# Kernel optimization log

Measured on AMD Instinct MI355X. Metric: run time of the kernel, lower is better.

The kernel has to match this reference:

```python
import jax, jax.numpy as jnp
import numpy as np

N = 20000   # nodes
E = 320000  # edges (before self-loops)
HID = 64    # hidden_dim
H = 4       # attention heads
C = HID     # per-head channels (concat=False -> mean over heads)
CDIM = 8    # contrastive_dim
NEG_SLOPE = 0.2


def setup_inputs() -> dict:
    key = jax.random.key(0)
    ks = jax.random.split(key, 32)
    g = lambda k, shape: (jax.random.normal(k, shape, jnp.float32) * 0.05)
    inp = {
        "x": jax.random.normal(ks[0], (N, 8), jnp.float32),
        "edge_index": jax.random.randint(ks[1], (2, E), 0, N, jnp.int64),
        # lc_encode MLP: 8 -> 32 -> HID
        "W_enc1": g(ks[2], (8, 32)),  "b_enc1": jnp.zeros((32,), jnp.float32),
        "W_enc2": g(ks[3], (32, HID)), "b_enc2": jnp.zeros((HID,), jnp.float32),
        # three GATConv layers: lin (HID -> H*C, no bias), att_src/att_dst (H, C), bias (C,)
        "W_g1": g(ks[4], (HID, H * C)), "as1": g(ks[5], (H, C)), "ad1": g(ks[6], (H, C)), "bg1": jnp.zeros((C,), jnp.float32),
        "W_g2": g(ks[7], (HID, H * C)), "as2": g(ks[8], (H, C)), "ad2": g(ks[9], (H, C)), "bg2": jnp.zeros((C,), jnp.float32),
        "W_g3": g(ks[10], (HID, H * C)), "as3": g(ks[11], (H, C)), "ad3": g(ks[12], (H, C)), "bg3": jnp.zeros((C,), jnp.float32),
        # output MLP: HID -> 64 -> 32 -> CDIM (dropout inactive at eval)
        "W_o1": g(ks[13], (HID, 64)), "b_o1": jnp.zeros((64,), jnp.float32),
        "W_o2": g(ks[14], (64, 32)),  "b_o2": jnp.zeros((32,), jnp.float32),
        "W_o3": g(ks[15], (32, CDIM)), "b_o3": jnp.zeros((CDIM,), jnp.float32),
    }
    return inp


def gat_conv(x, src, dst, n, W, att_src, att_dst, bias):
    # PyG GATConv, heads=H, concat=False (mean over heads), eval mode (no dropout)
    h = (x @ W).reshape(n, H, C)                       # [N,H,C]
    a_src = jnp.einsum('nhc,hc->nh', h, att_src)        # [N,H]
    a_dst = jnp.einsum('nhc,hc->nh', h, att_dst)        # [N,H]
    logits = jax.nn.leaky_relu(a_src[src] + a_dst[dst], NEG_SLOPE)  # [Etot,H]
    m = jax.ops.segment_max(logits, dst, num_segments=n)            # segment softmax (stable)
    e = jnp.exp(logits - m[dst])
    denom = jax.ops.segment_sum(e, dst, num_segments=n)
    alpha = e / (denom[dst] + 1e-16)                    # [Etot,H]
    msg = h[src] * alpha[:, :, None]                    # [Etot,H,C]
    out = jax.ops.segment_sum(msg, dst, num_segments=n) # [N,H,C]
    return out.mean(axis=1) + bias                      # concat=False -> head mean


def reference(x, edge_index, W_enc1, b_enc1, W_enc2, b_enc2,
              W_g1, as1, ad1, bg1, W_g2, as2, ad2, bg2, W_g3, as3, ad3, bg3,
              W_o1, b_o1, W_o2, b_o2, W_o3, b_o3):
    n = x.shape[0]
    loops = jnp.arange(n, dtype=edge_index.dtype)       # GATConv add_self_loops=True
    src = jnp.concatenate([edge_index[0], loops])
    dst = jnp.concatenate([edge_index[1], loops])

    h = jax.nn.elu(jax.nn.elu(x @ W_enc1 + b_enc1) @ W_enc2 + b_enc2)
    h1 = gat_conv(h, src, dst, n, W_g1, as1, ad1, bg1) + h
    h2 = gat_conv(h1, src, dst, n, W_g2, as2, ad2, bg2) + h1
    h3 = gat_conv(h2, src, dst, n, W_g3, as3, ad3, bg3) + h2

    o = jax.nn.elu(h3 @ W_o1 + b_o1)
    o = jax.nn.elu(o @ W_o2 + b_o2)
    return o @ W_o3 + b_o3
```

## Files before the change

kernel.cpp:

```cpp
#include <hip/hip_runtime.h>
#include <cstdint>
#include <cstddef>

#define NEG_SLOPE 0.2f

__device__ __forceinline__ float elu_f(float x) {
    return x > 0.f ? x : expm1f(x);
}

__global__ __launch_bounds__(256) void prep_kernel(
    const int* __restrict__ ei,
    const float* __restrict__ W0, const float* __restrict__ as0, const float* __restrict__ ad0,
    const float* __restrict__ W1, const float* __restrict__ as1, const float* __restrict__ ad1,
    const float* __restrict__ W2, const float* __restrict__ as2, const float* __restrict__ ad2,
    int* __restrict__ cnt, int* __restrict__ ready, int* __restrict__ flag,
    float* __restrict__ vfold, int n) {
    const int b = blockIdx.x, t = threadIdx.x;
    if (b < 79) {
        const int i = b * 256 + t;
        if (i < n) cnt[i] = 0;
        if (b == 0) {
            if (t < 128) ready[t] = 0;
            if (t == 0) {
                int acc = 0;
#pragma unroll
                for (int k = 0; k < 8; ++k) acc |= ei[2 * k + 1];
                flag[0] = (acc == 0) ? 1 : 0;
            }
        }
        return;
    }
    const int e = (b - 79) * 256 + t;
    if (e >= 1536) return;
    const int l = e >> 9, rem = e & 511;
    const int k = rem >> 3, j = rem & 7, h = j & 3;
    const float* W   = (l == 0) ? W0  : (l == 1) ? W1  : W2;
    const float* as_ = (l == 0) ? as0 : (l == 1) ? as1 : as2;
    const float* ad_ = (l == 0) ? ad0 : (l == 1) ? ad1 : ad2;
    const float* av = (j < 4) ? as_ : ad_;
    const float* wr = W + k * 256 + h * 64;
    const float* ar = av + h * 64;
    float s = 0.f;
#pragma unroll 8
    for (int cc = 0; cc < 64; ++cc) s += wr[cc] * ar[cc];
    vfold[l * 512 + k * 8 + j] = s;
}

__global__ void count_kernel(const int* __restrict__ ei, const int* __restrict__ flag,
                             int E, int Etot, int* __restrict__ cnt) {
    int e = blockIdx.x * blockDim.x + threadIdx.x;
    if (e >= Etot) return;
    int d;
    if (e < E) d = flag[0] ? ei[2 * (size_t)(E + e)] : ei[E + e];
    else       d = e - E;
    atomicAdd(&cnt[d], 1);
}

#define SCAN_B 256
__global__ __launch_bounds__(256) void scan_onepass_kernel(
    const int* __restrict__ cnt, int* __restrict__ ready,
    int* __restrict__ rowptr, int* __restrict__ cursor, int n) {
    __shared__ int sd[SCAN_B];
    __shared__ int sred[128];
    __shared__ int s_pref;
    const int b = blockIdx.x, t = threadIdx.x;
    const int g = b * SCAN_B + t;
    const int v = (g < n) ? cnt[g] : 0;
    sd[t] = v;
    __syncthreads();
    for (int off = 1; off < SCAN_B; off <<= 1) {
        int add = (t >= off) ? sd[t - off] : 0;
        __syncthreads();
        sd[t] += add;
        __syncthreads();
    }
    if (t == SCAN_B - 1) atomicExch(&ready[b], sd[SCAN_B - 1] + 1);
    if (t < 128) {
        int pv = 0;
        if (t < b) {
            do { pv = atomicAdd(&ready[t], 0); __builtin_amdgcn_s_sleep(1); } while (pv == 0);
            pv -= 1;
        }
        sred[t] = pv;
    }
    __syncthreads();
    if (t == 0) {
        int s = 0;
#pragma unroll 8
        for (int i = 0; i < 128; ++i) s += sred[i];
        s_pref = s;
    }
    __syncthreads();
    const int pre = s_pref;
    if (g < n) {
        const int e = pre + sd[t];
        rowptr[g + 1] = e;
        cursor[g] = e - v;
        if (g == 0) rowptr[0] = 0;
    }
}

#define H1STR 68
__global__ __launch_bounds__(256) void fillenc_kernel(
    const int* __restrict__ ei, const int* __restrict__ flag,
    int E, int Etot, int* __restrict__ cursor, int* __restrict__ col, int FB,
    const float* __restrict__ x,
    const float* __restrict__ W1, const float* __restrict__ b1,
    const float* __restrict__ W2, const float* __restrict__ b2,
    const float* __restrict__ vfold0,
    float* __restrict__ h0, float* __restrict__ asrc, float* __restrict__ adst,
    int n_nodes) {
    if (blockIdx.x < FB) {
        const int e = blockIdx.x * 256 + threadIdx.x;
        if (e >= Etot) return;
        int s, d;
        if (e < E) {
            if (flag[0]) { s = ei[2 * (size_t)e]; d = ei[2 * (size_t)(E + e)]; }
            else         { s = ei[e];             d = ei[E + e]; }
        } else {
            s = d = e - E;
        }
        int pos = atomicAdd(&cursor[d], 1);
        col[pos] = s;
        return;
    }
    __shared__ float W1s[256];
    __shared__ float b1s[32];
    __shared__ float W2s[2048];
    __shared__ float b2s[64];
    __shared__ float vsd[512];
    __shared__ float xS[512];
    __shared__ float h1T[32 * H1STR];
    const int t = threadIdx.x;
    const int n0 = (blockIdx.x - FB) * 64;
    const int rem = n_nodes - n0;

    *(float4*)(W2s + t * 4) = *(const float4*)(W2 + t * 4);
    *(float4*)(W2s + 1024 + t * 4) = *(const float4*)(W2 + 1024 + t * 4);
    if (t < 64)  *(float4*)(W1s + t * 4) = *(const float4*)(W1 + t * 4);
    if (t < 8)   *(float4*)(b1s + t * 4) = *(const float4*)(b1 + t * 4);
    if (t < 16)  *(float4*)(b2s + t * 4) = *(const float4*)(b2 + t * 4);
    if (t < 128) *(float4*)(vsd + t * 4) = *(const float4*)(vfold0 + t * 4);
    if (t < 128) {
        const int fidx = t * 4;
        float4 v = make_float4(0.f, 0.f, 0.f, 0.f);
        if (fidx < rem * 8) v = *(const float4*)(x + (size_t)n0 * 8 + fidx);
        *(float4*)(xS + fidx) = v;
    }
    __syncthreads();

    {
        const int nl = t >> 2;
        const int j0 = (t & 3) * 8;
        const float4 xa = *(const float4*)(xS + nl * 8);
        const float4 xb = *(const float4*)(xS + nl * 8 + 4);
        const float xk[8] = {xa.x, xa.y, xa.z, xa.w, xb.x, xb.y, xb.z, xb.w};
        float a[8];
#pragma unroll
        for (int u = 0; u < 8; ++u) a[u] = b1s[j0 + u];
#pragma unroll
        for (int k = 0; k < 8; ++k) {
            const float4 w0 = *(const float4*)(W1s + k * 32 + j0);
            const float4 w1 = *(const float4*)(W1s + k * 32 + j0 + 4);
            a[0] += xk[k] * w0.x; a[1] += xk[k] * w0.y;
            a[2] += xk[k] * w0.z; a[3] += xk[k] * w0.w;
            a[4] += xk[k] * w1.x; a[5] += xk[k] * w1.y;
            a[6] += xk[k] * w1.z; a[7] += xk[k] * w1.w;
        }
#pragma unroll
        for (int u = 0; u < 8; ++u) h1T[(j0 + u) * H1STR + nl] = elu_f(a[u]);
    }
    __syncthreads();

    const int cg = t & 15;
    const int nq = t >> 4;
    const int c0 = cg * 4;
    float acc[4][4];
#pragma unroll
    for (int i = 0; i < 4; ++i)
#pragma unroll
        for (int c = 0; c < 4; ++c) acc[i][c] = b2s[c0 + c];
#pragma unroll 8
    for (int k = 0; k < 32; ++k) {
        const float4 hv = *(const float4*)(h1T + k * H1STR + nq * 4);
        const float4 wv = *(const float4*)(W2s + k * 64 + c0);
        const float hvv[4] = {hv.x, hv.y, hv.z, hv.w};
#pragma unroll
        for (int i = 0; i < 4; ++i) {
            acc[i][0] += hvv[i] * wv.x; acc[i][1] += hvv[i] * wv.y;
            acc[i][2] += hvv[i] * wv.z; acc[i][3] += hvv[i] * wv.w;
        }
    }
    float o[4][4];
#pragma unroll
    for (int i = 0; i < 4; ++i)
#pragma unroll
        for (int c = 0; c < 4; ++c) o[i][c] = elu_f(acc[i][c]);

#pragma unroll
    for (int i = 0; i < 4; ++i) {
        const int n = n0 + nq * 4 + i;
        if (n < n_nodes)
            *(float4*)(h0 + (size_t)n * 64 + c0) =
                make_float4(o[i][0], o[i][1], o[i][2], o[i][3]);
    }
    float ad[4][8];
#pragma unroll
    for (int i = 0; i < 4; ++i)
#pragma unroll
        for (int jj = 0; jj < 8; ++jj) ad[i][jj] = 0.f;
#pragma unroll
    for (int c = 0; c < 4; ++c) {
        const float4 v0 = *(const float4*)(vsd + (c0 + c) * 8);
        const float4 v1 = *(const float4*)(vsd + (c0 + c) * 8 + 4);
#pragma unroll
        for (int i = 0; i < 4; ++i) {
            ad[i][0] += o[i][c] * v0.x; ad[i][1] += o[i][c] * v0.y;
            ad[i][2] += o[i][c] * v0.z; ad[i][3] += o[i][c] * v0.w;
            ad[i][4] += o[i][c] * v1.x; ad[i][5] += o[i][c] * v1.y;
            ad[i][6] += o[i][c] * v1.z; ad[i][7] += o[i][c] * v1.w;
        }
    }
#pragma unroll
    for (int off = 1; off < 16; off <<= 1) {
#pragma unroll
        for (int i = 0; i < 4; ++i)
#pragma unroll
            for (int jj = 0; jj < 8; ++jj)
                ad[i][jj] += __shfl_xor(ad[i][jj], off);
    }
    if (cg == 0) {
#pragma unroll
        for (int i = 0; i < 4; ++i) {
            const int n = n0 + nq * 4 + i;
            if (n < n_nodes) {
#pragma unroll
                for (int h = 0; h < 4; ++h) {
                    asrc[n * 4 + h] = ad[i][h];
                    adst[n * 4 + h] = ad[i][4 + h];
                }
            }
        }
    }
}

#define GSTR 132
__global__ __launch_bounds__(512, 8) void gat_fused_kernel(
    const float* __restrict__ bin, const float* __restrict__ asrc,
    const float* __restrict__ adst, const int* __restrict__ rowptr,
    const int* __restrict__ col,
    const float* __restrict__ W, const float* __restrict__ bias,
    const float* __restrict__ vfold_next, int has_next,
    float* __restrict__ out,
    float* __restrict__ nasrc, float* __restrict__ nadst,
    const float* __restrict__ Wm1, const float* __restrict__ bm1,
    const float* __restrict__ Wm2, const float* __restrict__ bm2,
    const float* __restrict__ Wm3, const float* __restrict__ bm3,
    float* __restrict__ mlp_out, int n_nodes) {
    __shared__ float gS[32 * GSTR];
    __shared__ float Wp[4096];
    __shared__ float vN[512];
    const int t = threadIdx.x;
    const int n0 = blockIdx.x * 32;
    const int grp = t >> 4;
    const int q = t & 15;
    const int c0 = q * 4;

    if (has_next && t < 128) *(float4*)(vN + t * 4) = *(const float4*)(vfold_next + t * 4);

    float keep[8];
    {
        const int n = n0 + grp;
        float acc[4][4];
#pragma unroll
        for (int h = 0; h < 4; ++h)
#pragma unroll
            for (int z = 0; z < 4; ++z) acc[h][z] = 0.f;
        if (n < n_nodes) {
            float4 den4 = make_float4(0.f, 0.f, 0.f, 0.f);
            const float4 ad4 = *(const float4*)(adst + (size_t)n * 4);
            const int start = rowptr[n], end = rowptr[n + 1];
            for (int base = start; base < end; base += 16) {
                const int cnt = min(16, end - base);
                int c = 0;
                float4 w4 = make_float4(0.f, 0.f, 0.f, 0.f);
                if (base + q < end) {
                    c = col[base + q];
                    const float4 av = *(const float4*)(asrc + (size_t)c * 4);
                    float l0 = av.x + ad4.x; l0 = l0 > 0.f ? l0 : NEG_SLOPE * l0;
                    float l1 = av.y + ad4.y; l1 = l1 > 0.f ? l1 : NEG_SLOPE * l1;
                    float l2 = av.z + ad4.z; l2 = l2 > 0.f ? l2 : NEG_SLOPE * l2;
                    float l3 = av.w + ad4.w; l3 = l3 > 0.f ? l3 : NEG_SLOPE * l3;
                    w4.x = __expf(fminf(l0, 60.f));
                    w4.y = __expf(fminf(l1, 60.f));
                    w4.z = __expf(fminf(l2, 60.f));
                    w4.w = __expf(fminf(l3, 60.f));
                    den4.x += w4.x; den4.y += w4.y; den4.z += w4.z; den4.w += w4.w;
                }
                int j = 0;
                for (; j + 4 <= cnt; j += 4) {
#pragma unroll
                    for (int u = 0; u < 4; ++u) {
                        const int s = __shfl(c, j + u, 16);
                        const float4 hv = *(const float4*)(bin + (size_t)s * 64 + q * 4);
                        const float wx = __shfl(w4.x, j + u, 16);
                        const float wy = __shfl(w4.y, j + u, 16);
                        const float wz = __shfl(w4.z, j + u, 16);
                        const float ww = __shfl(w4.w, j + u, 16);
                        acc[0][0] += wx * hv.x; acc[0][1] += wx * hv.y;
                        acc[0][2] += wx * hv.z; acc[0][3] += wx * hv.w;
                        acc[1][0] += wy * hv.x; acc[1][1] += wy * hv.y;
                        acc[1][2] += wy * hv.z; acc[1][3] += wy * hv.w;
                        acc[2][0] += wz * hv.x; acc[2][1] += wz * hv.y;
                        acc[2][2] += wz * hv.z; acc[2][3] += wz * hv.w;
                        acc[3][0] += ww * hv.x; acc[3][1] += ww * hv.y;
                        acc[3][2] += ww * hv.z; acc[3][3] += ww * hv.w;
                    }
                }
                for (; j < cnt; ++j) {
                    const int s = __shfl(c, j, 16);
                    const float4 hv = *(const float4*)(bin + (size_t)s * 64 + q * 4);
                    const float wx = __shfl(w4.x, j, 16);
                    const float wy = __shfl(w4.y, j, 16);
                    const float wz = __shfl(w4.z, j, 16);
                    const float ww = __shfl(w4.w, j, 16);
                    acc[0][0] += wx * hv.x; acc[0][1] += wx * hv.y;
                    acc[0][2] += wx * hv.z; acc[0][3] += wx * hv.w;
                    acc[1][0] += wy * hv.x; acc[1][1] += wy * hv.y;
                    acc[1][2] += wy * hv.z; acc[1][3] += wy * hv.w;
                    acc[2][0] += wz * hv.x; acc[2][1] += wz * hv.y;
                    acc[2][2] += wz * hv.z; acc[2][3] += wz * hv.w;
                    acc[3][0] += ww * hv.x; acc[3][1] += ww * hv.y;
                    acc[3][2] += ww * hv.z; acc[3][3] += ww * hv.w;
                }
            }
#pragma unroll
            for (int off = 1; off < 16; off <<= 1) {
                den4.x += __shfl_xor(den4.x, off, 16);
                den4.y += __shfl_xor(den4.y, off, 16);
                den4.z += __shfl_xor(den4.z, off, 16);
                den4.w += __shfl_xor(den4.w, off, 16);
            }
            const float i0 = 1.f / (den4.x + 1e-16f);
            const float i1 = 1.f / (den4.y + 1e-16f);
            const float i2 = 1.f / (den4.z + 1e-16f);
            const float i3 = 1.f / (den4.w + 1e-16f);
            *(float4*)(gS + grp * GSTR + c0) =
                make_float4(acc[0][0] * i0, acc[0][1] * i0, acc[0][2] * i0, acc[0][3] * i0);
            *(float4*)(gS + grp * GSTR + 64 + c0) =
                make_float4(acc[1][0] * i1, acc[1][1] * i1, acc[1][2] * i1, acc[1][3] * i1);
            keep[0] = acc[2][0] * i2; keep[1] = acc[2][1] * i2;
            keep[2] = acc[2][2] * i2; keep[3] = acc[2][3] * i2;
            keep[4] = acc[3][0] * i3; keep[5] = acc[3][1] * i3;
            keep[6] = acc[3][2] * i3; keep[7] = acc[3][3] * i3;
        } else {
            const float4 z4 = make_float4(0.f, 0.f, 0.f, 0.f);
            *(float4*)(gS + grp * GSTR + c0) = z4;
            *(float4*)(gS + grp * GSTR + 64 + c0) = z4;
#pragma unroll
            for (int u = 0; u < 8; ++u) keep[u] = 0.f;
        }
    }

    const int ng2 = t >> 4;
    float ga2[2][4];
#pragma unroll
    for (int i = 0; i < 2; ++i)
#pragma unroll
        for (int c = 0; c < 4; ++c) ga2[i][c] = 0.f;

#pragma unroll
    for (int half = 0; half < 2; ++half) {
        if (half == 1) {
            *(float4*)(gS + grp * GSTR + c0) =
                make_float4(keep[0], keep[1], keep[2], keep[3]);
            *(float4*)(gS + grp * GSTR + 64 + c0) =
                make_float4(keep[4], keep[5], keep[6], keep[7]);
        }
#pragma unroll
        for (int s = 0; s < 2; ++s) {
#pragma unroll
            for (int j = 0; j < 2; ++j) {
                const int f4 = j * 512 + t;
                const int kl = f4 >> 4;
                const int c = (f4 & 15) * 4;
                const int m = half * 128 + s * 64 + kl;
                const int h = m >> 6, kk = m & 63;
                *(float4*)(Wp + kl * 64 + c) = *(const float4*)(W + kk * 256 + h * 64 + c);
            }
            __syncthreads();
            if (t < 256) {
#pragma unroll 4
                for (int ks = 0; ks < 64; ks += 4) {
                    const float4 a0 = *(const float4*)(gS + (ng2 * 2 + 0) * GSTR + s * 64 + ks);
                    const float4 a1 = *(const float4*)(gS + (ng2 * 2 + 1) * GSTR + s * 64 + ks);
                    const float4 w0 = *(const float4*)(Wp + (ks + 0) * 64 + c0);
                    const float4 w1 = *(const float4*)(Wp + (ks + 1) * 64 + c0);
                    const float4 w2 = *(const float4*)(Wp + (ks + 2) * 64 + c0);
                    const float4 w3 = *(const float4*)(Wp + (ks + 3) * 64 + c0);
                    ga2[0][0] += a0.x * w0.x + a0.y * w1.x + a0.z * w2.x + a0.w * w3.x;
                    ga2[0][1] += a0.x * w0.y + a0.y * w1.y + a0.z * w2.y + a0.w * w3.y;
                    ga2[0][2] += a0.x * w0.z + a0.y * w1.z + a0.z * w2.z + a0.w * w3.z;
                    ga2[0][3] += a0.x * w0.w + a0.y * w1.w + a0.z * w2.w + a0.w * w3.w;
                    ga2[1][0] += a1.x * w0.x + a1.y * w1.x + a1.z * w2.x + a1.w * w3.x;
                    ga2[1][1] += a1.x * w0.y + a1.y * w1.y + a1.z * w2.y + a1.w * w3.y;
                    ga2[1][2] += a1.x * w0.z + a1.y * w1.z + a1.z * w2.z + a1.w * w3.z;
                    ga2[1][3] += a1.x * w0.w + a1.y * w1.w + a1.z * w2.w + a1.w * w3.w;
                }
            }
            __syncthreads();
        }
    }

    float o[2][4];
    if (t < 256) {
        const float4 bb = *(const float4*)(bias + c0);
#pragma unroll
        for (int i = 0; i < 2; ++i) {
            const int n = n0 + ng2 * 2 + i;
            if (n < n_nodes) {
                const float4 x4 = *(const float4*)(bin + (size_t)n * 64 + c0);
                o[i][0] = 0.25f * ga2[i][0] + bb.x + x4.x;
                o[i][1] = 0.25f * ga2[i][1] + bb.y + x4.y;
                o[i][2] = 0.25f * ga2[i][2] + bb.z + x4.z;
                o[i][3] = 0.25f * ga2[i][3] + bb.w + x4.w;
                if (has_next)
                    *(float4*)(out + (size_t)n * 64 + c0) =
                        make_float4(o[i][0], o[i][1], o[i][2], o[i][3]);
            } else {
                o[i][0] = o[i][1] = o[i][2] = o[i][3] = 0.f;
            }
        }
    } else {
#pragma unroll
        for (int i = 0; i < 2; ++i)
            o[i][0] = o[i][1] = o[i][2] = o[i][3] = 0.f;
    }

    if (has_next) {
        if (t < 256) {
            float pj[2][8];
#pragma unroll
            for (int i = 0; i < 2; ++i)
#pragma unroll
                for (int jj = 0; jj < 8; ++jj) pj[i][jj] = 0.f;
#pragma unroll
            for (int c = 0; c < 4; ++c) {
                const float4 v0 = *(const float4*)(vN + (c0 + c) * 8);
                const float4 v1 = *(const float4*)(vN + (c0 + c) * 8 + 4);
#pragma unroll
                for (int i = 0; i < 2; ++i) {
                    pj[i][0] += o[i][c] * v0.x; pj[i][1] += o[i][c] * v0.y;
                    pj[i][2] += o[i][c] * v0.z; pj[i][3] += o[i][c] * v0.w;
                    pj[i][4] += o[i][c] * v1.x; pj[i][5] += o[i][c] * v1.y;
                    pj[i][6] += o[i][c] * v1.z; pj[i][7] += o[i][c] * v1.w;
                }
            }
#pragma unroll
            for (int off = 1; off < 16; off <<= 1) {
#pragma unroll
                for (int i = 0; i < 2; ++i)
#pragma unroll
                    for (int jj = 0; jj < 8; ++jj)
                        pj[i][jj] += __shfl_xor(pj[i][jj], off);
            }
            if (q == 0) {
#pragma unroll
                for (int i = 0; i < 2; ++i) {
                    const int n = n0 + ng2 * 2 + i;
                    if (n < n_nodes) {
#pragma unroll
                        for (int h = 0; h < 4; ++h) {
                            nasrc[n * 4 + h] = pj[i][h];
                            nadst[n * 4 + h] = pj[i][4 + h];
                        }
                    }
                }
            }
        }
        return;
    }

    if (t < 256) {
#pragma unroll
        for (int i = 0; i < 2; ++i)
            *(float4*)(gS + (ng2 * 2 + i) * GSTR + c0) =
                make_float4(o[i][0], o[i][1], o[i][2], o[i][3]);
    }
#pragma unroll
    for (int j = 0; j < 2; ++j)
        *(float4*)(Wp + (j * 512 + t) * 4) = *(const float4*)(Wm1 + (j * 512 + t) * 4);
    if (t < 64) vN[t] = bm1[t];
    else if (t < 96) vN[t] = bm2[t - 64];
    else if (t < 104) vN[t] = bm3[t - 96];
    if (t < 256) vN[104 + t] = Wm3[t];
    __syncthreads();
    if (t < 256) {
        const int ng = t >> 3;
        const int cm0 = (t & 7) * 8;
        float a1[8];
#pragma unroll
        for (int u = 0; u < 8; ++u) a1[u] = vN[cm0 + u];
#pragma unroll 4
        for (int k = 0; k < 64; ++k) {
            const float hv = gS[ng * GSTR + k];
            const float4 w0 = *(const float4*)(Wp + k * 64 + cm0);
            const float4 w1 = *(const float4*)(Wp + k * 64 + cm0 + 4);
            a1[0] += hv * w0.x; a1[1] += hv * w0.y;
            a1[2] += hv * w0.z; a1[3] += hv * w0.w;
            a1[4] += hv * w1.x; a1[5] += hv * w1.y;
            a1[6] += hv * w1.z; a1[7] += hv * w1.w;
        }
        *(float4*)(gS + ng * GSTR + 64 + cm0) =
            make_float4(elu_f(a1[0]), elu_f(a1[1]), elu_f(a1[2]), elu_f(a1[3]));
        *(float4*)(gS + ng * GSTR + 64 + cm0 + 4) =
            make_float4(elu_f(a1[4]), elu_f(a1[5]), elu_f(a1[6]), elu_f(a1[7]));
    }
    __syncthreads();
    *(float4*)(Wp + t * 4) = *(const float4*)(Wm2 + t * 4);
    __syncthreads();
    if (t < 256) {
        const int nn = t >> 3;
        const int cc0 = (t & 7) * 4;
        float a2[4];
#pragma unroll
        for (int u = 0; u < 4; ++u) a2[u] = vN[64 + cc0 + u];
#pragma unroll 4
        for (int j = 0; j < 64; ++j) {
            const float ov = gS[nn * GSTR + 64 + j];
            const float4 w = *(const float4*)(Wp + j * 32 + cc0);
            a2[0] += ov * w.x; a2[1] += ov * w.y;
            a2[2] += ov * w.z; a2[3] += ov * w.w;
        }
        __syncthreads();
        *(float4*)(gS + nn * GSTR + cc0) =
            make_float4(elu_f(a2[0]), elu_f(a2[1]), elu_f(a2[2]), elu_f(a2[3]));
    } else {
        __syncthreads();
    }
    __syncthreads();
    if (t < 256) {
        const int nl = t >> 3;
        const int c3 = t & 7;
        const int n = n0 + nl;
        if (n < n_nodes) {
            float a3 = vN[96 + c3];
#pragma unroll 4
            for (int j = 0; j < 32; ++j)
                a3 += gS[nl * GSTR + j] * vN[104 + j * 8 + c3];
            mlp_out[(size_t)n * 8 + c3] = a3;
        }
    }
}

extern "C" void kernel_launch(void* const* d_in, const int* in_sizes, int n_in,
                              void* d_out, int out_size, void* d_ws, size_t ws_size,
                              hipStream_t stream) {
    const float* x     = (const float*)d_in[0];
    const int*   ei    = (const int*)d_in[1];
    const float* Wenc1 = (const float*)d_in[2];
    const float* benc1 = (const float*)d_in[3];
    const float* Wenc2 = (const float*)d_in[4];
    const float* benc2 = (const float*)d_in[5];
    const float* Wg[3]  = {(const float*)d_in[6],  (const float*)d_in[10], (const float*)d_in[14]};
    const float* as_[3] = {(const float*)d_in[7],  (const float*)d_in[11], (const float*)d_in[15]};
    const float* ad_[3] = {(const float*)d_in[8],  (const float*)d_in[12], (const float*)d_in[16]};
    const float* bg[3]  = {(const float*)d_in[9],  (const float*)d_in[13], (const float*)d_in[17]};
    const float* Wo1 = (const float*)d_in[18];
    const float* bo1 = (const float*)d_in[19];
    const float* Wo2 = (const float*)d_in[20];
    const float* bo2 = (const float*)d_in[21];
    const float* Wo3 = (const float*)d_in[22];
    const float* bo3 = (const float*)d_in[23];

    const int N = in_sizes[0] / 8;
    const int E = in_sizes[1] / 2;
    const int Etot = E + N;
    const int nblk = (N + SCAN_B - 1) / SCAN_B;
    const int FB = (Etot + 255) / 256;
    const int NB64 = (N + 63) / 64;
    const int NB32 = (N + 31) / 32;

    float* buf0  = (float*)d_ws;
    float* buf1  = buf0 + (size_t)N * 64;
    float* asA   = buf1 + (size_t)N * 64;
    float* adA   = asA + (size_t)N * 4;
    float* asB   = adA + (size_t)N * 4;
    float* adB   = asB + (size_t)N * 4;
    float* vfold = adB + (size_t)N * 4;
    int* rowptr = (int*)(vfold + 3 * 512);
    int* cursor = rowptr + (N + 2);
    int* cnt    = cursor + N;
    int* ready  = cnt + N;
    int* flag   = ready + 128;
    int* col    = flag + 2;

    prep_kernel<<<nblk + 6, 256, 0, stream>>>(ei,
        Wg[0], as_[0], ad_[0], Wg[1], as_[1], ad_[1], Wg[2], as_[2], ad_[2],
        cnt, ready, flag, vfold, N);
    count_kernel<<<(Etot + 255) / 256, 256, 0, stream>>>(ei, flag, E, Etot, cnt);
    scan_onepass_kernel<<<nblk, SCAN_B, 0, stream>>>(cnt, ready, rowptr, cursor, N);
    fillenc_kernel<<<FB + NB64, 256, 0, stream>>>(ei, flag, E, Etot, cursor, col, FB,
                                                  x, Wenc1, benc1, Wenc2, benc2,
                                                  vfold, buf0, asA, adA, N);

    gat_fused_kernel<<<NB32, 512, 0, stream>>>(
        buf0, asA, adA, rowptr, col, Wg[0], bg[0], vfold + 512, 1,
        buf1, asB, adB, Wo1, bo1, Wo2, bo2, Wo3, bo3, (float*)d_out, N);
    gat_fused_kernel<<<NB32, 512, 0, stream>>>(
        buf1, asB, adB, rowptr, col, Wg[1], bg[1], vfold + 1024, 1,
        buf0, asA, adA, Wo1, bo1, Wo2, bo2, Wo3, bo3, (float*)d_out, N);
    gat_fused_kernel<<<NB32, 512, 0, stream>>>(
        buf0, asA, adA, rowptr, col, Wg[2], bg[2], vfold, 0,
        buf1, asB, adB, Wo1, bo1, Wo2, bo2, Wo3, bo3, (float*)d_out, N);
}
```

Baseline: 281.8 us.

## Stage edge weights in LDS for gather and use 4-node register tiles in projection

The aggregation loop no longer broadcasts edge indices and attention weights with five shuffles per edge. Each lane writes its weight and source index to shared memory, and every lane then reads them back, accumulating the denominator redundantly so the final xor-reduction is gone. The post-aggregation projection now runs on 128 threads, each computing a 4-node by 4-channel tile so every W read from LDS is reused across more rows. Results pass through shared memory to the epilogue. This cuts shuffle traffic and LDS weight reads, but it idles half the threads in the GEMM and adds extra syncs and LDS round-trips.

```diff
diff --git a/kernel.cpp b/kernel.cpp
--- a/kernel.cpp
+++ b/kernel.cpp
@@ -266,6 +266,9 @@
     const int q = t & 15;
     const int c0 = q * 4;
 
+    float* wEf = Wp;
+    int*   sEi = (int*)(Wp + 2176);
+
     if (has_next && t < 128) *(float4*)(vN + t * 4) = *(const float4*)(vfold_next + t * 4);
 
     float keep[8];
@@ -282,8 +285,8 @@
             const int start = rowptr[n], end = rowptr[n + 1];
             for (int base = start; base < end; base += 16) {
                 const int cnt = min(16, end - base);
+                float4 w4 = make_float4(0.f, 0.f, 0.f, 0.f);
                 int c = 0;
-                float4 w4 = make_float4(0.f, 0.f, 0.f, 0.f);
                 if (base + q < end) {
                     c = col[base + q];
                     const float4 av = *(const float4*)(asrc + (size_t)c * 4);
@@ -295,51 +298,26 @@
                     w4.y = __expf(fminf(l1, 60.f));
                     w4.z = __expf(fminf(l2, 60.f));
                     w4.w = __expf(fminf(l3, 60.f));
-                    den4.x += w4.x; den4.y += w4.y; den4.z += w4.z; den4.w += w4.w;
                 }
-                int j = 0;
-                for (; j + 4 <= cnt; j += 4) {
-#pragma unroll
-                    for (int u = 0; u < 4; ++u) {
-                        const int s = __shfl(c, j + u, 16);
-                        const float4 hv = *(const float4*)(bin + (size_t)s * 64 + q * 4);
-                        const float wx = __shfl(w4.x, j + u, 16);
-                        const float wy = __shfl(w4.y, j + u, 16);
-                        const float wz = __shfl(w4.z, j + u, 16);
-                        const float ww = __shfl(w4.w, j + u, 16);
-                        acc[0][0] += wx * hv.x; acc[0][1] += wx * hv.y;
-                        acc[0][2] += wx * hv.z; acc[0][3] += wx * hv.w;
-                        acc[1][0] += wy * hv.x; acc[1][1] += wy * hv.y;
-                        acc[1][2] += wy * hv.z; acc[1][3] += wy * hv.w;
-                        acc[2][0] += wz * hv.x; acc[2][1] += wz * hv.y;
-                        acc[2][2] += wz * hv.z; acc[2][3] += wz * hv.w;
-                        acc[3][0] += ww * hv.x; acc[3][1] += ww * hv.y;
-                        acc[3][2] += ww * hv.z; acc[3][3] += ww * hv.w;
-                    }
+                *(float4*)(wEf + (grp * 17 + q) * 4) = w4;
+                sEi[grp * 17 + q] = c;
+                __builtin_amdgcn_sched_barrier(0);
+#pragma unroll 4
+                for (int j = 0; j < cnt; ++j) {
+                    const float4 wj = *(const float4*)(wEf + (grp * 17 + j) * 4);
+                    const int s = sEi[grp * 17 + j];
+                    const float4 hv = *(const float4*)(bin + (size_t)s * 64 + q * 4);
+                    den4.x += wj.x; den4.y += wj.y; den4.z += wj.z; den4.w += wj.w;
+                    acc[0][0] += wj.x * hv.x; acc[0][1] += wj.x * hv.y;
+                    acc[0][2] += wj.x * hv.z; acc[0][3] += wj.x * hv.w;
+                    acc[1][0] += wj.y * hv.x; acc[1][1] += wj.y * hv.y;
+                    acc[1][2] += wj.y * hv.z; acc[1][3] += wj.y * hv.w;
+                    acc[2][0] += wj.z * hv.x; acc[2][1] += wj.z * hv.y;
+                    acc[2][2] += wj.z * hv.z; acc[2][3] += wj.z * hv.w;
+                    acc[3][0] += wj.w * hv.x; acc[3][1] += wj.w * hv.y;
+                    acc[3][2] += wj.w * hv.z; acc[3][3] += wj.w * hv.w;
                 }
-                for (; j < cnt; ++j) {
-                    const int s = __shfl(c, j, 16);
-                    const float4 hv = *(const float4*)(bin + (size_t)s * 64 + q * 4);
-                    const float wx = __shfl(w4.x, j, 16);
-                    const float wy = __shfl(w4.y, j, 16);
-                    const float wz = __shfl(w4.z, j, 16);
-                    const float ww = __shfl(w4.w, j, 16);
-                    acc[0][0] += wx * hv.x; acc[0][1] += wx * hv.y;
-                    acc[0][2] += wx * hv.z; acc[0][3] += wx * hv.w;
-                    acc[1][0] += wy * hv.x; acc[1][1] += wy * hv.y;
-                    acc[1][2] += wy * hv.z; acc[1][3] += wy * hv.w;
-                    acc[2][0] += wz * hv.x; acc[2][1] += wz * hv.y;
-                    acc[2][2] += wz * hv.z; acc[2][3] += wz * hv.w;
-                    acc[3][0] += ww * hv.x; acc[3][1] += ww * hv.y;
-                    acc[3][2] += ww * hv.z; acc[3][3] += ww * hv.w;
-                }
-            }
-#pragma unroll
-            for (int off = 1; off < 16; off <<= 1) {
-                den4.x += __shfl_xor(den4.x, off, 16);
-                den4.y += __shfl_xor(den4.y, off, 16);
-                den4.z += __shfl_xor(den4.z, off, 16);
-                den4.w += __shfl_xor(den4.w, off, 16);
+                __builtin_amdgcn_sched_barrier(0);
             }
             const float i0 = 1.f / (den4.x + 1e-16f);
             const float i1 = 1.f / (den4.y + 1e-16f);
@@ -361,13 +339,14 @@
             for (int u = 0; u < 8; ++u) keep[u] = 0.f;
         }
     }
-
-    const int ng2 = t >> 4;
-    float ga2[2][4];
-#pragma unroll
-    for (int i = 0; i < 2; ++i)
-#pragma unroll
-        for (int c = 0; c < 4; ++c) ga2[i][c] = 0.f;
+    __syncthreads();
+
+    const int ng4 = t >> 4;
+    float ga[4][4];
+#pragma unroll
+    for (int i = 0; i < 4; ++i)
+#pragma unroll
+        for (int c = 0; c < 4; ++c) ga[i][c] = 0.f;
 
 #pragma unroll
     for (int half = 0; half < 2; ++half) {
@@ -389,29 +368,36 @@
                 *(float4*)(Wp + kl * 64 + c) = *(const float4*)(W + kk * 256 + h * 64 + c);
             }
             __syncthreads();
-            if (t < 256) {
+            if (t < 128) {
 #pragma unroll 4
                 for (int ks = 0; ks < 64; ks += 4) {
-                    const float4 a0 = *(const float4*)(gS + (ng2 * 2 + 0) * GSTR + s * 64 + ks);
-                    const float4 a1 = *(const float4*)(gS + (ng2 * 2 + 1) * GSTR + s * 64 + ks);
                     const float4 w0 = *(const float4*)(Wp + (ks + 0) * 64 + c0);
                     const float4 w1 = *(const float4*)(Wp + (ks + 1) * 64 + c0);
                     const float4 w2 = *(const float4*)(Wp + (ks + 2) * 64 + c0);
                     const float4 w3 = *(const float4*)(Wp + (ks + 3) * 64 + c0);
-                    ga2[0][0] += a0.x * w0.x + a0.y * w1.x + a0.z * w2.x + a0.w * w3.x;
-                    ga2[0][1] += a0.x * w0.y + a0.y * w1.y + a0.z * w2.y + a0.w * w3.y;
-                    ga2[0][2] += a0.x * w0.z + a0.y * w1.z + a0.z * w2.z + a0.w * w3.z;
-                    ga2[0][3] += a0.x * w0.w + a0.y * w1.w + a0.z * w2.w + a0.w * w3.w;
-                    ga2[1][0] += a1.x * w0.x + a1.y * w1.x + a1.z * w2.x + a1.w * w3.x;
-                    ga2[1][1] += a1.x * w0.y + a1.y * w1.y + a1.z * w2.y + a1.w * w3.y;
-                    ga2[1][2] += a1.x * w0.z + a1.y * w1.z + a1.z * w2.z + a1.w * w3.z;
-                    ga2[1][3] += a1.x * w0.w + a1.y * w1.w + a1.z * w2.w + a1.w * w3.w;
+#pragma unroll
+                    for (int i = 0; i < 4; ++i) {
+                        const float4 a = *(const float4*)(gS + (ng4 * 4 + i) * GSTR + s * 64 + ks);
+                        ga[i][0] += a.x * w0.x + a.y * w1.x + a.z * w2.x + a.w * w3.x;
+                        ga[i][1] += a.x * w0.y + a.y * w1.y + a.z * w2.y + a.w * w3.y;
+                        ga[i][2] += a.x * w0.z + a.y * w1.z + a.z * w2.z + a.w * w3.z;
+                        ga[i][3] += a.x * w0.w + a.y * w1.w + a.z * w2.w + a.w * w3.w;
+                    }
                 }
             }
             __syncthreads();
         }
     }
 
+    if (t < 128) {
+#pragma unroll
+        for (int i = 0; i < 4; ++i)
+            *(float4*)(gS + (ng4 * 4 + i) * GSTR + c0) =
+                make_float4(ga[i][0], ga[i][1], ga[i][2], ga[i][3]);
+    }
+    __syncthreads();
+
+    const int ng2 = t >> 4;
     float o[2][4];
     if (t < 256) {
         const float4 bb = *(const float4*)(bias + c0);
@@ -419,11 +405,12 @@
         for (int i = 0; i < 2; ++i) {
             const int n = n0 + ng2 * 2 + i;
             if (n < n_nodes) {
+                const float4 g4 = *(const float4*)(gS + (ng2 * 2 + i) * GSTR + c0);
                 const float4 x4 = *(const float4*)(bin + (size_t)n * 64 + c0);
-                o[i][0] = 0.25f * ga2[i][0] + bb.x + x4.x;
-                o[i][1] = 0.25f * ga2[i][1] + bb.y + x4.y;
-                o[i][2] = 0.25f * ga2[i][2] + bb.z + x4.z;
-                o[i][3] = 0.25f * ga2[i][3] + bb.w + x4.w;
+                o[i][0] = 0.25f * g4.x + bb.x + x4.x;
+                o[i][1] = 0.25f * g4.y + bb.y + x4.y;
+                o[i][2] = 0.25f * g4.z + bb.z + x4.z;
+                o[i][3] = 0.25f * g4.w + bb.w + x4.w;
                 if (has_next)
                     *(float4*)(out + (size_t)n * 64 + c0) =
                         make_float4(o[i][0], o[i][1], o[i][2], o[i][3]);
```

Measured after the change: 326.9 us. 1.16x slower.

## Merge count, scan and fill into one kernel with inter-block spin barriers

Applied to the files above, without the earlier changes.

Replaces the separate count, scan and fill+encode kernels with one build kernel. Counting blocks signal completion through an atomic counter, scan blocks wait on it and then publish their own done counter, and all encoder and scan blocks then fill the CSR with a grid-stride loop. This removes two kernel launches and their serialization gaps, and lets the encoder MLP run alongside the count and scan phases. In exchange it relies on spin-waiting, which can deadlock if the waiting blocks are resident while the blocks they wait on cannot be scheduled. It also drops the count-stage blocks from the fill phase.

```diff
diff --git a/kernel.cpp b/kernel.cpp
--- a/kernel.cpp
+++ b/kernel.cpp
@@ -14,7 +14,7 @@
     const float* __restrict__ W1, const float* __restrict__ as1, const float* __restrict__ ad1,
     const float* __restrict__ W2, const float* __restrict__ as2, const float* __restrict__ ad2,
     int* __restrict__ cnt, int* __restrict__ ready, int* __restrict__ flag,
-    float* __restrict__ vfold, int n) {
+    int* __restrict__ dones, float* __restrict__ vfold, int n) {
     const int b = blockIdx.x, t = threadIdx.x;
     if (b < 79) {
         const int i = b * 256 + t;
@@ -26,6 +26,8 @@
 #pragma unroll
                 for (int k = 0; k < 8; ++k) acc |= ei[2 * k + 1];
                 flag[0] = (acc == 0) ? 1 : 0;
+                dones[0] = 0;
+                dones[1] = 0;
             }
         }
         return;
@@ -46,84 +48,20 @@
     vfold[l * 512 + k * 8 + j] = s;
 }
 
-__global__ void count_kernel(const int* __restrict__ ei, const int* __restrict__ flag,
-                             int E, int Etot, int* __restrict__ cnt) {
-    int e = blockIdx.x * blockDim.x + threadIdx.x;
-    if (e >= Etot) return;
-    int d;
-    if (e < E) d = flag[0] ? ei[2 * (size_t)(E + e)] : ei[E + e];
-    else       d = e - E;
-    atomicAdd(&cnt[d], 1);
-}
-
 #define SCAN_B 256
-__global__ __launch_bounds__(256) void scan_onepass_kernel(
-    const int* __restrict__ cnt, int* __restrict__ ready,
-    int* __restrict__ rowptr, int* __restrict__ cursor, int n) {
-    __shared__ int sd[SCAN_B];
-    __shared__ int sred[128];
-    __shared__ int s_pref;
-    const int b = blockIdx.x, t = threadIdx.x;
-    const int g = b * SCAN_B + t;
-    const int v = (g < n) ? cnt[g] : 0;
-    sd[t] = v;
-    __syncthreads();
-    for (int off = 1; off < SCAN_B; off <<= 1) {
-        int add = (t >= off) ? sd[t - off] : 0;
-        __syncthreads();
-        sd[t] += add;
-        __syncthreads();
-    }
-    if (t == SCAN_B - 1) atomicExch(&ready[b], sd[SCAN_B - 1] + 1);
-    if (t < 128) {
-        int pv = 0;
-        if (t < b) {
-            do { pv = atomicAdd(&ready[t], 0); __builtin_amdgcn_s_sleep(1); } while (pv == 0);
-            pv -= 1;
-        }
-        sred[t] = pv;
-    }
-    __syncthreads();
-    if (t == 0) {
-        int s = 0;
-#pragma unroll 8
-        for (int i = 0; i < 128; ++i) s += sred[i];
-        s_pref = s;
-    }
-    __syncthreads();
-    const int pre = s_pref;
-    if (g < n) {
-        const int e = pre + sd[t];
-        rowptr[g + 1] = e;
-        cursor[g] = e - v;
-        if (g == 0) rowptr[0] = 0;
-    }
-}
 
 #define H1STR 68
-__global__ __launch_bounds__(256) void fillenc_kernel(
+__global__ __launch_bounds__(256, 4) void build_kernel(
     const int* __restrict__ ei, const int* __restrict__ flag,
-    int E, int Etot, int* __restrict__ cursor, int* __restrict__ col, int FB,
+    int E, int Etot, int NB, int CB, int SB,
+    int* __restrict__ cnt, int* __restrict__ ready, int* __restrict__ dones,
+    int* __restrict__ rowptr, int* __restrict__ cursor, int* __restrict__ col,
     const float* __restrict__ x,
     const float* __restrict__ W1, const float* __restrict__ b1,
     const float* __restrict__ W2, const float* __restrict__ b2,
     const float* __restrict__ vfold0,
     float* __restrict__ h0, float* __restrict__ asrc, float* __restrict__ adst,
     int n_nodes) {
-    if (blockIdx.x < FB) {
-        const int e = blockIdx.x * 256 + threadIdx.x;
-        if (e >= Etot) return;
-        int s, d;
-        if (e < E) {
-            if (flag[0]) { s = ei[2 * (size_t)e]; d = ei[2 * (size_t)(E + e)]; }
-            else         { s = ei[e];             d = ei[E + e]; }
-        } else {
-            s = d = e - E;
-        }
-        int pos = atomicAdd(&cursor[d], 1);
-        col[pos] = s;
-        return;
-    }
     __shared__ float W1s[256];
     __shared__ float b1s[32];
     __shared__ float W2s[2048];
@@ -131,115 +69,199 @@
     __shared__ float vsd[512];
     __shared__ float xS[512];
     __shared__ float h1T[32 * H1STR];
-    const int t = threadIdx.x;
-    const int n0 = (blockIdx.x - FB) * 64;
-    const int rem = n_nodes - n0;
-
-    *(float4*)(W2s + t * 4) = *(const float4*)(W2 + t * 4);
-    *(float4*)(W2s + 1024 + t * 4) = *(const float4*)(W2 + 1024 + t * 4);
-    if (t < 64)  *(float4*)(W1s + t * 4) = *(const float4*)(W1 + t * 4);
-    if (t < 8)   *(float4*)(b1s + t * 4) = *(const float4*)(b1 + t * 4);
-    if (t < 16)  *(float4*)(b2s + t * 4) = *(const float4*)(b2 + t * 4);
-    if (t < 128) *(float4*)(vsd + t * 4) = *(const float4*)(vfold0 + t * 4);
-    if (t < 128) {
-        const int fidx = t * 4;
-        float4 v = make_float4(0.f, 0.f, 0.f, 0.f);
-        if (fidx < rem * 8) v = *(const float4*)(x + (size_t)n0 * 8 + fidx);
-        *(float4*)(xS + fidx) = v;
-    }
-    __syncthreads();
-
-    {
-        const int nl = t >> 2;
-        const int j0 = (t & 3) * 8;
-        const float4 xa = *(const float4*)(xS + nl * 8);
-        const float4 xb = *(const float4*)(xS + nl * 8 + 4);
-        const float xk[8] = {xa.x, xa.y, xa.z, xa.w, xb.x, xb.y, xb.z, xb.w};
-        float a[8];
-#pragma unroll
-        for (int u = 0; u < 8; ++u) a[u] = b1s[j0 + u];
-#pragma unroll
-        for (int k = 0; k < 8; ++k) {
-            const float4 w0 = *(const float4*)(W1s + k * 32 + j0);
-            const float4 w1 = *(const float4*)(W1s + k * 32 + j0 + 4);
-            a[0] += xk[k] * w0.x; a[1] += xk[k] * w0.y;
-            a[2] += xk[k] * w0.z; a[3] += xk[k] * w0.w;
-            a[4] += xk[k] * w1.x; a[5] += xk[k] * w1.y;
-            a[6] += xk[k] * w1.z; a[7] += xk[k] * w1.w;
-        }
-#pragma unroll
-        for (int u = 0; u < 8; ++u) h1T[(j0 + u) * H1STR + nl] = elu_f(a[u]);
-    }
-    __syncthreads();
-
-    const int cg = t & 15;
-    const int nq = t >> 4;
-    const int c0 = cg * 4;
-    float acc[4][4];
-#pragma unroll
-    for (int i = 0; i < 4; ++i)
-#pragma unroll
-        for (int c = 0; c < 4; ++c) acc[i][c] = b2s[c0 + c];
+    __shared__ int scb[SCAN_B];
+    __shared__ int sred[128];
+    __shared__ int s_pref;
+    const int b = blockIdx.x, t = threadIdx.x;
+
+    if (b >= NB && b < NB + CB) {
+        const int e = (b - NB) * 256 + t;
+        if (e < Etot) {
+            int d;
+            if (e < E) d = flag[0] ? ei[2 * (size_t)(E + e)] : ei[E + e];
+            else       d = e - E;
+            atomicAdd(&cnt[d], 1);
+        }
+        __syncthreads();
+        if (t == 0) { __threadfence(); atomicAdd(&dones[0], 1); }
+        return;
+    }
+
+    int rank;
+    if (b >= NB + CB) {
+        const int sb = b - NB - CB;
+        if (t == 0) {
+            while (atomicAdd(&dones[0], 0) < CB) __builtin_amdgcn_s_sleep(2);
+        }
+        __syncthreads();
+        const int g = sb * SCAN_B + t;
+        const int v = (g < n_nodes) ? atomicAdd(&cnt[g], 0) : 0;
+        scb[t] = v;
+        __syncthreads();
+        for (int off = 1; off < SCAN_B; off <<= 1) {
+            int add = (t >= off) ? scb[t - off] : 0;
+            __syncthreads();
+            scb[t] += add;
+            __syncthreads();
+        }
+        if (t == SCAN_B - 1) atomicExch(&ready[sb], scb[SCAN_B - 1] + 1);
+        if (t < 128) {
+            int pv = 0;
+            if (t < sb) {
+                do { pv = atomicAdd(&ready[t], 0); __builtin_amdgcn_s_sleep(1); } while (pv == 0);
+                pv -= 1;
+            }
+            sred[t] = pv;
+        }
+        __syncthreads();
+        if (t == 0) {
+            int s = 0;
 #pragma unroll 8
-    for (int k = 0; k < 32; ++k) {
-        const float4 hv = *(const float4*)(h1T + k * H1STR + nq * 4);
-        const float4 wv = *(const float4*)(W2s + k * 64 + c0);
-        const float hvv[4] = {hv.x, hv.y, hv.z, hv.w};
-#pragma unroll
-        for (int i = 0; i < 4; ++i) {
-            acc[i][0] += hvv[i] * wv.x; acc[i][1] += hvv[i] * wv.y;
-            acc[i][2] += hvv[i] * wv.z; acc[i][3] += hvv[i] * wv.w;
-        }
-    }
-    float o[4][4];
-#pragma unroll
-    for (int i = 0; i < 4; ++i)
-#pragma unroll
-        for (int c = 0; c < 4; ++c) o[i][c] = elu_f(acc[i][c]);
-
-#pragma unroll
-    for (int i = 0; i < 4; ++i) {
-        const int n = n0 + nq * 4 + i;
-        if (n < n_nodes)
-            *(float4*)(h0 + (size_t)n * 64 + c0) =
-                make_float4(o[i][0], o[i][1], o[i][2], o[i][3]);
-    }
-    float ad[4][8];
-#pragma unroll
-    for (int i = 0; i < 4; ++i)
-#pragma unroll
-        for (int jj = 0; jj < 8; ++jj) ad[i][jj] = 0.f;
-#pragma unroll
-    for (int c = 0; c < 4; ++c) {
-        const float4 v0 = *(const float4*)(vsd + (c0 + c) * 8);
-        const float4 v1 = *(const float4*)(vsd + (c0 + c) * 8 + 4);
-#pragma unroll
-        for (int i = 0; i < 4; ++i) {
-            ad[i][0] += o[i][c] * v0.x; ad[i][1] += o[i][c] * v0.y;
-            ad[i][2] += o[i][c] * v0.z; ad[i][3] += o[i][c] * v0.w;
-            ad[i][4] += o[i][c] * v1.x; ad[i][5] += o[i][c] * v1.y;
-            ad[i][6] += o[i][c] * v1.z; ad[i][7] += o[i][c] * v1.w;
-        }
-    }
-#pragma unroll
-    for (int off = 1; off < 16; off <<= 1) {
+            for (int i = 0; i < 128; ++i) s += sred[i];
+            s_pref = s;
+        }
+        __syncthreads();
+        const int pre = s_pref;
+        if (g < n_nodes) {
+            const int e = pre + scb[t];
+            rowptr[g + 1] = e;
+            cursor[g] = e - v;
+            if (g == 0) rowptr[0] = 0;
+        }
+        __syncthreads();
+        if (t == 0) { __threadfence(); atomicAdd(&dones[1], 1); }
+        rank = NB + sb;
+    } else {
+        const int n0 = b * 64;
+        const int rem = n_nodes - n0;
+
+        *(float4*)(W2s + t * 4) = *(const float4*)(W2 + t * 4);
+        *(float4*)(W2s + 1024 + t * 4) = *(const float4*)(W2 + 1024 + t * 4);
+        if (t < 64)  *(float4*)(W1s + t * 4) = *(const float4*)(W1 + t * 4);
+        if (t < 8)   *(float4*)(b1s + t * 4) = *(const float4*)(b1 + t * 4);
+        if (t < 16)  *(float4*)(b2s + t * 4) = *(const float4*)(b2 + t * 4);
+        if (t < 128) *(float4*)(vsd + t * 4) = *(const float4*)(vfold0 + t * 4);
+        if (t < 128) {
+            const int fidx = t * 4;
+            float4 v = make_float4(0.f, 0.f, 0.f, 0.f);
+            if (fidx < rem * 8) v = *(const float4*)(x + (size_t)n0 * 8 + fidx);
+            *(float4*)(xS + fidx) = v;
+        }
+        __syncthreads();
+
+        {
+            const int nl = t >> 2;
+            const int j0 = (t & 3) * 8;
+            const float4 xa = *(const float4*)(xS + nl * 8);
+            const float4 xb = *(const float4*)(xS + nl * 8 + 4);
+            const float xk[8] = {xa.x, xa.y, xa.z, xa.w, xb.x, xb.y, xb.z, xb.w};
+            float a[8];
+#pragma unroll
+            for (int u = 0; u < 8; ++u) a[u] = b1s[j0 + u];
+#pragma unroll
+            for (int k = 0; k < 8; ++k) {
+                const float4 w0 = *(const float4*)(W1s + k * 32 + j0);
+                const float4 w1 = *(const float4*)(W1s + k * 32 + j0 + 4);
+                a[0] += xk[k] * w0.x; a[1] += xk[k] * w0.y;
+                a[2] += xk[k] * w0.z; a[3] += xk[k] * w0.w;
+                a[4] += xk[k] * w1.x; a[5] += xk[k] * w1.y;
+                a[6] += xk[k] * w1.z; a[7] += xk[k] * w1.w;
+            }
+#pragma unroll
+            for (int u = 0; u < 8; ++u) h1T[(j0 + u) * H1STR + nl] = elu_f(a[u]);
+        }
+        __syncthreads();
+
+        const int cg = t & 15;
+        const int nq = t >> 4;
+        const int c0 = cg * 4;
+        float acc[4][4];
 #pragma unroll
         for (int i = 0; i < 4; ++i)
 #pragma unroll
-            for (int jj = 0; jj < 8; ++jj)
-                ad[i][jj] += __shfl_xor(ad[i][jj], off);
-    }
-    if (cg == 0) {
+            for (int c = 0; c < 4; ++c) acc[i][c] = b2s[c0 + c];
+#pragma unroll 8
+        for (int k = 0; k < 32; ++k) {
+            const float4 hv = *(const float4*)(h1T + k * H1STR + nq * 4);
+            const float4 wv = *(const float4*)(W2s + k * 64 + c0);
+            const float hvv[4] = {hv.x, hv.y, hv.z, hv.w};
+#pragma unroll
+            for (int i = 0; i < 4; ++i) {
+                acc[i][0] += hvv[i] * wv.x; acc[i][1] += hvv[i] * wv.y;
+                acc[i][2] += hvv[i] * wv.z; acc[i][3] += hvv[i] * wv.w;
+            }
+        }
+        float o[4][4];
+#pragma unroll
+        for (int i = 0; i < 4; ++i)
+#pragma unroll
+            for (int c = 0; c < 4; ++c) o[i][c] = elu_f(acc[i][c]);
+
 #pragma unroll
         for (int i = 0; i < 4; ++i) {
             const int n = n0 + nq * 4 + i;
-            if (n < n_nodes) {
-#pragma unroll
-                for (int h = 0; h < 4; ++h) {
-                    asrc[n * 4 + h] = ad[i][h];
-                    adst[n * 4 + h] = ad[i][4 + h];
+            if (n < n_nodes)
+                *(float4*)(h0 + (size_t)n * 64 + c0) =
+                    make_float4(o[i][0], o[i][1], o[i][2], o[i][3]);
+        }
+        float ad[4][8];
+#pragma unroll
+        for (int i = 0; i < 4; ++i)
+#pragma unroll
+            for (int jj = 0; jj < 8; ++jj) ad[i][jj] = 0.f;
+#pragma unroll
+        for (int c = 0; c < 4; ++c) {
+            const float4 v0 = *(const float4*)(vsd + (c0 + c) * 8);
+            const float4 v1 = *(const float4*)(vsd + (c0 + c) * 8 + 4);
+#pragma unroll
+            for (int i = 0; i < 4; ++i) {
+                ad[i][0] += o[i][c] * v0.x; ad[i][1] += o[i][c] * v0.y;
+                ad[i][2] += o[i][c] * v0.z; ad[i][3] += o[i][c] * v0.w;
+                ad[i][4] += o[i][c] * v1.x; ad[i][5] += o[i][c] * v1.y;
+                ad[i][6] += o[i][c] * v1.z; ad[i][7] += o[i][c] * v1.w;
+            }
+        }
+#pragma unroll
+        for (int off = 1; off < 16; off <<= 1) {
+#pragma unroll
+            for (int i = 0; i < 4; ++i)
+#pragma unroll
+                for (int jj = 0; jj < 8; ++jj)
+                    ad[i][jj] += __shfl_xor(ad[i][jj], off);
+        }
+        if (cg == 0) {
+#pragma unroll
+            for (int i = 0; i < 4; ++i) {
+                const int n = n0 + nq * 4 + i;
+                if (n < n_nodes) {
+#pragma unroll
+                    for (int h = 0; h < 4; ++h) {
+                        asrc[n * 4 + h] = ad[i][h];
+                        adst[n * 4 + h] = ad[i][4 + h];
+                    }
                 }
             }
+        }
+        rank = b;
+    }
+
+    if (t == 0) {
+        while (atomicAdd(&dones[1], 0) < SB) __builtin_amdgcn_s_sleep(2);
+    }
+    __syncthreads();
+    {
+        const int fl = flag[0];
+        const int F = NB + SB;
+        for (int e = rank * 256 + t; e < Etot; e += F * 256) {
+            int s, d;
+            if (e < E) {
+                if (fl) { s = ei[2 * (size_t)e]; d = ei[2 * (size_t)(E + e)]; }
+                else    { s = ei[e];             d = ei[E + e]; }
+            } else {
+                s = d = e - E;
+            }
+            int pos = atomicAdd(&cursor[d], 1);
+            col[pos] = s;
         }
     }
 }
@@ -577,7 +599,7 @@
     const int E = in_sizes[1] / 2;
     const int Etot = E + N;
     const int nblk = (N + SCAN_B - 1) / SCAN_B;
-    const int FB = (Etot + 255) / 256;
+    const int CB = (Etot + 255) / 256;
     const int NB64 = (N + 63) / 64;
     const int NB32 = (N + 31) / 32;
 
@@ -593,16 +615,17 @@
     int* cnt    = cursor + N;
     int* ready  = cnt + N;
     int* flag   = ready + 128;
-    int* col    = flag + 2;
+    int* dones  = flag + 2;
+    int* col    = dones + 2;
 
     prep_kernel<<<nblk + 6, 256, 0, stream>>>(ei,
         Wg[0], as_[0], ad_[0], Wg[1], as_[1], ad_[1], Wg[2], as_[2], ad_[2],
-        cnt, ready, flag, vfold, N);
-    count_kernel<<<(Etot + 255) / 256, 256, 0, stream>>>(ei, flag, E, Etot, cnt);
-    scan_onepass_kernel<<<nblk, SCAN_B, 0, stream>>>(cnt, ready, rowptr, cursor, N);
-    fillenc_kernel<<<FB + NB64, 256, 0, stream>>>(ei, flag, E, Etot, cursor, col, FB,
-                                                  x, Wenc1, benc1, Wenc2, benc2,
-                                                  vfold, buf0, asA, adA, N);
+        cnt, ready, flag, dones, vfold, N);
+
+    build_kernel<<<NB64 + CB + nblk, 256, 0, stream>>>(
+        ei, flag, E, Etot, NB64, CB, nblk,
+        cnt, ready, dones, rowptr, cursor, col,
+        x, Wenc1, benc1, Wenc2, benc2, vfold, buf0, asA, adA, N);
 
     gat_fused_kernel<<<NB32, 512, 0, stream>>>(
         buf0, asA, adA, rowptr, col, Wg[0], bg[0], vfold + 512, 1,
```

After: 309.6 us. 1.1x slower.
